# Optimization experiments

Hardware: AMD Instinct MI355X
Metric: run time of the kernel (lower is better)

Reference implementation:

```python
import jax, jax.numpy as jnp
import numpy as np

NODE_DIM = 128
NUM_IRREPS = 224          # 128 + 64 + 32 gates (one per irrep channel)
SPH_DIM = 480             # 128*1 + 64*3 + 32*5
HIDDEN = NODE_DIM + 2 * NUM_IRREPS  # 576
NUM_BASIS = 20
N_NODES = 10000
N_EDGES = 160000
# Each gate scalar is broadcast over its irrep's (2l+1) components.
_REPEATS = np.array([1] * 128 + [3] * 64 + [5] * 32)


def _expand_gate(g):
    # [E, 224] -> [E, 480], repeating each gate over its irrep dimension
    return jnp.repeat(g, _REPEATS, axis=-1, total_repeat_length=SPH_DIM)


def setup_inputs() -> dict:
    key = jax.random.key(0)
    ks = jax.random.split(key, 12)
    x_scalar = jax.random.normal(ks[0], (N_NODES, NODE_DIM), dtype=jnp.float32)
    x_spherical = jax.random.normal(ks[1], (N_NODES, SPH_DIM), dtype=jnp.float32)
    rbf = jax.random.uniform(ks[2], (N_EDGES, NUM_BASIS), dtype=jnp.float32)
    fcut = jax.random.uniform(ks[3], (N_EDGES, 1), dtype=jnp.float32)
    rsh = jax.random.normal(ks[4], (N_EDGES, SPH_DIM), dtype=jnp.float32)
    edge_index = jax.random.randint(ks[5], (2, N_EDGES), 0, N_NODES, dtype=jnp.int64)
    s1 = 1.0 / np.sqrt(NODE_DIM)
    s2 = 1.0 / np.sqrt(NUM_BASIS)
    W1 = jax.random.uniform(ks[6], (NODE_DIM, NODE_DIM), jnp.float32, -s1, s1)
    b1 = jnp.zeros((NODE_DIM,), jnp.float32)
    W2 = jax.random.uniform(ks[7], (NODE_DIM, HIDDEN), jnp.float32, -s1, s1)
    b2 = jnp.zeros((HIDDEN,), jnp.float32)
    Wr = jax.random.uniform(ks[8], (NUM_BASIS, HIDDEN), jnp.float32, -s2, s2)
    br = jnp.zeros((HIDDEN,), jnp.float32)
    return {"x_scalar": x_scalar, "x_spherical": x_spherical, "rbf": rbf,
            "fcut": fcut, "rsh": rsh, "edge_index": edge_index,
            "W1": W1, "b1": b1, "W2": W2, "b2": b2, "Wr": Wr, "br": br}


def reference(x_scalar, x_spherical, rbf, fcut, rsh, edge_index,
              W1, b1, W2, b2, Wr, br):
    src, dst = edge_index[0], edge_index[1]
    # scalar MLP: Linear -> SiLU -> Linear
    scalar_out = jax.nn.silu(x_scalar @ W1 + b1) @ W2 + b2          # [N, 576]
    filter_weight = (rbf @ Wr + br) * fcut                          # [E, 576]
    filter_out = scalar_out[dst] * filter_weight                    # [E, 576]
    gate_state = filter_out[:, :NUM_IRREPS]                         # [E, 224]
    gate_edge = filter_out[:, NUM_IRREPS:2 * NUM_IRREPS]            # [E, 224]
    message_scalar = filter_out[:, 2 * NUM_IRREPS:]                 # [E, 128]
    # ElementwiseTensorProduct(edge_irreps, '224x0e'): per-channel scalar gating
    message_spherical = (x_spherical[dst] * _expand_gate(gate_state)
                         + rsh * _expand_gate(gate_edge))           # [E, 480]
    new_scalar = x_scalar.at[src].add(message_scalar)
    new_spherical = x_spherical.at[src].add(message_spherical)
    return (new_scalar, new_spherical)
```

## Files before the change

kernel.cpp:

```cpp
#include <hip/hip_runtime.h>

#define NODE_DIM 128
#define NUM_IRREPS 224
#define SPH_DIM 480
#define HIDDEN 576
#define NUM_BASIS 20
#define N_NODES 10000
#define N_EDGES 160000
#define NPB 4
#define EB 16
#define NT 36
#define IRP 233
#define SCP 138
#define SOP 577
#define PREP_BLOCKS 2048
#define MLP_BLOCKS ((N_NODES + NPB - 1) / NPB)

typedef __attribute__((ext_vector_type(8))) short short8v;
typedef __attribute__((ext_vector_type(4))) float f32x4;

__device__ __forceinline__ unsigned short f2bf(float f) {
    unsigned int u = __builtin_bit_cast(unsigned int, f);
    u = (u + 0x7fff + ((u >> 16) & 1)) >> 16;
    return (unsigned short)u;
}
__device__ __forceinline__ float bf2f(unsigned short h) {
    unsigned int u = ((unsigned int)h) << 16;
    return __builtin_bit_cast(float, u);
}

__global__ __launch_bounds__(256) void prep_mlp_kernel(
    const float* __restrict__ xs, const float* __restrict__ xsp,
    float* __restrict__ out,
    const int* __restrict__ eidx, int* __restrict__ counts,
    const float* __restrict__ Wr, unsigned short* __restrict__ bfrag,
    const float* __restrict__ W1, const float* __restrict__ b1,
    const float* __restrict__ W2, const float* __restrict__ b2,
    unsigned short* __restrict__ so_bf)
{
    const int t = threadIdx.x;
    if (blockIdx.x < PREP_BLOCKS) {
        const int stride = PREP_BLOCKS * 256;
        const int gt = blockIdx.x * 256 + t;
        for (int i = gt; i < N_NODES * NODE_DIM; i += stride) out[i] = xs[i];
        float* o2 = out + (size_t)N_NODES * NODE_DIM;
        for (int i = gt; i < N_NODES * SPH_DIM; i += stride) o2[i] = xsp[i];
        if (gt < N_EDGES) atomicAdd(&counts[eidx[gt]], 1);
        if (blockIdx.x == PREP_BLOCKS - 1) {
            for (int idx = t; idx < NT * 64; idx += 256) {
                const int nt = idx >> 6, l = idx & 63;
                const int col = nt * 16 + (l & 15);
                const int kb = (l >> 4) * 8;
                #pragma unroll
                for (int j = 0; j < 8; ++j) {
                    const int k = kb + j;
                    bfrag[(size_t)idx * 8 + j] = (k < NUM_BASIS) ? f2bf(Wr[k * HIDDEN + col]) : (unsigned short)0;
                }
            }
        }
        return;
    }
    __shared__ float xsm[NPB][NODE_DIM];
    __shared__ float hsm[NPB][NODE_DIM];
    const int n0 = (blockIdx.x - PREP_BLOCKS) * NPB;
    const int half = t >> 7;
    const int tc = t & 127;

    #pragma unroll
    for (int i = 0; i < 2; ++i) {
        const int nn = 2 * half + i;
        const int node = n0 + nn;
        xsm[nn][tc] = (node < N_NODES) ? xs[(size_t)node * NODE_DIM + tc] : 0.f;
    }
    __syncthreads();

    float acc[2] = {b1[tc], b1[tc]};
    for (int k = 0; k < NODE_DIM; ++k) {
        const float w = W1[k * NODE_DIM + tc];
        #pragma unroll
        for (int i = 0; i < 2; ++i) acc[i] = fmaf(xsm[2 * half + i][k], w, acc[i]);
    }
    #pragma unroll
    for (int i = 0; i < 2; ++i) {
        const float v = acc[i];
        hsm[2 * half + i][tc] = v / (1.f + __expf(-v));
    }
    __syncthreads();

    for (int j = t; j < HIDDEN; j += 256) {
        float a2[NPB];
        #pragma unroll
        for (int n = 0; n < NPB; ++n) a2[n] = b2[j];
        for (int k = 0; k < NODE_DIM; ++k) {
            const float w = W2[k * HIDDEN + j];
            #pragma unroll
            for (int n = 0; n < NPB; ++n) a2[n] = fmaf(hsm[n][k], w, a2[n]);
        }
        #pragma unroll
        for (int n = 0; n < NPB; ++n) {
            const int node = n0 + n;
            if (node < N_NODES) so_bf[(size_t)node * HIDDEN + j] = f2bf(a2[n]);
        }
    }
}

__global__ __launch_bounds__(1024) void scan_kernel(const int* __restrict__ counts,
                                                    int* __restrict__ offsets,
                                                    int* __restrict__ cursor) {
    __shared__ int wsum[16];
    const int tid = threadIdx.x;
    int vals[10];
    int run = 0;
    #pragma unroll
    for (int i = 0; i < 10; ++i) {
        int idx = tid * 10 + i;
        int c = (idx < N_NODES) ? counts[idx] : 0;
        vals[i] = run;
        run += c;
    }
    const int lane = tid & 63, w = tid >> 6;
    int inc = run;
    #pragma unroll
    for (int off = 1; off < 64; off <<= 1) {
        int v = __shfl_up(inc, off);
        if (lane >= off) inc += v;
    }
    if (lane == 63) wsum[w] = inc;
    __syncthreads();
    if (w == 0) {
        int v = (lane < 16) ? wsum[lane] : 0;
        #pragma unroll
        for (int off = 1; off < 16; off <<= 1) {
            int u = __shfl_up(v, off);
            if (lane >= off) v += u;
        }
        if (lane < 16) wsum[lane] = v;
    }
    __syncthreads();
    const int wbase = (w > 0) ? wsum[w - 1] : 0;
    const int base = wbase + inc - run;
    #pragma unroll
    for (int i = 0; i < 10; ++i) {
        int idx = tid * 10 + i;
        if (idx < N_NODES) {
            int v = base + vals[i];
            offsets[idx] = v;
            cursor[idx] = v;
        }
    }
    if (tid == 1023) offsets[N_NODES] = wbase + inc;
}

__global__ __launch_bounds__(256) void scatter_kernel(const int* __restrict__ eidx,
                                                      int* __restrict__ cursor,
                                                      int* __restrict__ edge_order,
                                                      int* __restrict__ edge_src) {
    int i = blockIdx.x * blockDim.x + threadIdx.x;
    if (i < N_EDGES) {
        int s = eidx[i];
        int pos = atomicAdd(&cursor[s], 1);
        edge_order[pos] = i;
        edge_src[pos] = s;
    }
}

__device__ __forceinline__ int gate_of(int d) {
    return (d < 128) ? d : (d < 320) ? (128 + (d - 128) / 3) : (192 + (d - 320) / 5);
}

__global__ __launch_bounds__(256, 4) void edge_mfma(
    const float* __restrict__ xsp,
    const float* __restrict__ rbf, const float* __restrict__ fcut,
    const float* __restrict__ rsh, const int* __restrict__ eidx,
    const unsigned short* __restrict__ bfrag, const float* __restrict__ br,
    const unsigned short* __restrict__ so_bf,
    const int* __restrict__ edge_order, const int* __restrict__ edge_src,
    float* __restrict__ out_scalar, float* __restrict__ out_sph)
{
    __shared__ unsigned short so_s[EB][SOP];
    __shared__ unsigned int   pair_s[EB][IRP];
    __shared__ unsigned short scal_s[EB][SCP];
    __shared__ float rbf_s[EB][NUM_BASIS];
    __shared__ int   e_s[EB];
    __shared__ int   src_s[EB];
    __shared__ int   dst_s[EB];
    __shared__ float fc_s[EB];

    const int t = threadIdx.x;
    const int base = blockIdx.x * EB;
    const int lane = t & 63, w = t >> 6;

    if (t < EB) {
        int pos = base + t;
        int e = edge_order[pos];
        e_s[t]   = e;
        src_s[t] = edge_src[pos];
        dst_s[t] = eidx[N_EDGES + e];
        fc_s[t]  = fcut[e];
    }
    __syncthreads();

    for (int i = t; i < EB * HIDDEN; i += 256) {
        const int row = i / HIDDEN, col = i - row * HIDDEN;
        so_s[row][col] = so_bf[(size_t)dst_s[row] * HIDDEN + col];
    }
    for (int i = t; i < EB * NUM_BASIS; i += 256) {
        const int row = i / NUM_BASIS, k = i - row * NUM_BASIS;
        rbf_s[row][k] = rbf[(size_t)e_s[row] * NUM_BASIS + k];
    }
    __syncthreads();

    const int m_row = lane & 15;
    const int kb = (lane >> 4) * 8;
    short8v a0;
    #pragma unroll
    for (int j = 0; j < 8; ++j) {
        const int k = kb + j;
        a0[j] = (k < NUM_BASIS) ? (short)f2bf(rbf_s[m_row][k]) : (short)0;
    }

    {
        const int rbase = (lane >> 4) * 4;
        float fA[4];
        #pragma unroll
        for (int r = 0; r < 4; ++r) fA[r] = fc_s[rbase + r];
        #pragma unroll
        for (int i = 0; i < NT / 4; ++i) {
            const int nt = w * (NT / 4) + i;
            const short8v bf = *(const short8v*)(bfrag + (size_t)(nt * 64 + lane) * 8);
            f32x4 c0 = {0.f, 0.f, 0.f, 0.f};
            c0 = __builtin_amdgcn_mfma_f32_16x16x32_bf16(a0, bf, c0, 0, 0, 0);
            const int col = nt * 16 + (lane & 15);
            const float brc = br[col];
            #pragma unroll
            for (int r = 0; r < 4; ++r) {
                const int row = rbase + r;
                const float sov = bf2f(so_s[row][col]);
                const float v = (c0[r] + brc) * fA[r] * sov;
                const unsigned short hv = f2bf(v);
                if (col < NUM_IRREPS) {
                    ((unsigned short*)&pair_s[row][col])[0] = hv;
                } else if (col < 2 * NUM_IRREPS) {
                    ((unsigned short*)&pair_s[row][col - NUM_IRREPS])[1] = hv;
                } else {
                    scal_s[row][col - 2 * NUM_IRREPS] = hv;
                }
            }
        }
    }
    __syncthreads();

    const bool sphOn = (t < 240);
    const int d0 = 2 * t;
    const int g0 = sphOn ? gate_of(d0) : 0;
    const int g1 = sphOn ? gate_of(d0 + 1) : 0;

    float accS = 0.f, accD0 = 0.f, accD1 = 0.f;
    int cur_src = src_s[0];

    #pragma unroll
    for (int le = 0; le < EB; ++le) {
        const int s = src_s[le];
        if (s != cur_src) {
            if (sphOn) {
                atomicAdd(&out_sph[(size_t)cur_src * SPH_DIM + d0],     accD0);
                atomicAdd(&out_sph[(size_t)cur_src * SPH_DIM + d0 + 1], accD1);
            }
            if (t < 128) atomicAdd(&out_scalar[(size_t)cur_src * NODE_DIM + t], accS);
            accD0 = accD1 = accS = 0.f;
            cur_src = s;
        }
        if (sphOn) {
            const float2 xv = *(const float2*)(xsp + (size_t)dst_s[le] * SPH_DIM + d0);
            const float2 rv = *(const float2*)(rsh + (size_t)e_s[le]  * SPH_DIM + d0);
            const unsigned int p0 = pair_s[le][g0];
            const unsigned int p1 = pair_s[le][g1];
            accD0 = fmaf(xv.x, bf2f((unsigned short)(p0 & 0xffffu)),
                    fmaf(rv.x, bf2f((unsigned short)(p0 >> 16)), accD0));
            accD1 = fmaf(xv.y, bf2f((unsigned short)(p1 & 0xffffu)),
                    fmaf(rv.y, bf2f((unsigned short)(p1 >> 16)), accD1));
        }
        if (t < 128) accS += bf2f(scal_s[le][t]);
    }
    if (sphOn) {
        atomicAdd(&out_sph[(size_t)cur_src * SPH_DIM + d0],     accD0);
        atomicAdd(&out_sph[(size_t)cur_src * SPH_DIM + d0 + 1], accD1);
    }
    if (t < 128) atomicAdd(&out_scalar[(size_t)cur_src * NODE_DIM + t], accS);
}

extern "C" void kernel_launch(void* const* d_in, const int* in_sizes, int n_in,
                              void* d_out, int out_size, void* d_ws, size_t ws_size,
                              hipStream_t stream) {
    const float* x_scalar    = (const float*)d_in[0];
    const float* x_spherical = (const float*)d_in[1];
    const float* rbf         = (const float*)d_in[2];
    const float* fcut        = (const float*)d_in[3];
    const float* rsh         = (const float*)d_in[4];
    const int*   eidx        = (const int*)d_in[5];
    const float* W1          = (const float*)d_in[6];
    const float* b1          = (const float*)d_in[7];
    const float* W2          = (const float*)d_in[8];
    const float* b2          = (const float*)d_in[9];
    const float* Wr          = (const float*)d_in[10];
    const float* br          = (const float*)d_in[11];

    float* out        = (float*)d_out;
    float* out_scalar = out;
    float* out_sph    = out + (size_t)N_NODES * NODE_DIM;

    unsigned short* so_bf   = (unsigned short*)d_ws;
    int*   counts     = (int*)(so_bf + (size_t)N_NODES * HIDDEN);
    int*   offsets    = counts + N_NODES;
    int*   cursor     = offsets + N_NODES + 1;
    int*   edge_order = cursor + N_NODES;
    int*   edge_src   = edge_order + N_EDGES;
    unsigned short* bfrag = (unsigned short*)((((uintptr_t)(edge_src + N_EDGES)) + 15) & ~(uintptr_t)15);

    hipMemsetAsync(counts, 0, N_NODES * sizeof(int), stream);
    prep_mlp_kernel<<<PREP_BLOCKS + MLP_BLOCKS, 256, 0, stream>>>(
        x_scalar, x_spherical, out, eidx, counts, Wr, bfrag,
        W1, b1, W2, b2, so_bf);
    scan_kernel<<<1, 1024, 0, stream>>>(counts, offsets, cursor);
    scatter_kernel<<<(N_EDGES + 255) / 256, 256, 0, stream>>>(eidx, cursor, edge_order, edge_src);
    edge_mfma<<<N_EDGES / EB, 256, 0, stream>>>(x_spherical, rbf, fcut, rsh, eidx,
                                                bfrag, br, so_bf, edge_order, edge_src,
                                                out_scalar, out_sph);
}
```

Measured before the change: 336.0 us.

## Switch edge kernel to per-node gather, dropping output copy and atomics

```diff
diff --git a/kernel.cpp b/kernel.cpp
--- a/kernel.cpp
+++ b/kernel.cpp
@@ -12,8 +12,7 @@
 #define NT 36
 #define IRP 233
 #define SCP 138
-#define SOP 577
-#define PREP_BLOCKS 2048
+#define PREP_BLOCKS 625
 #define MLP_BLOCKS ((N_NODES + NPB - 1) / NPB)
 
 typedef __attribute__((ext_vector_type(8))) short short8v;
@@ -28,10 +27,12 @@
     unsigned int u = ((unsigned int)h) << 16;
     return __builtin_bit_cast(float, u);
 }
+__device__ __forceinline__ int gate_of(int d) {
+    return (d < 128) ? d : (d < 320) ? (128 + (d - 128) / 3) : (192 + (d - 320) / 5);
+}
 
 __global__ __launch_bounds__(256) void prep_mlp_kernel(
-    const float* __restrict__ xs, const float* __restrict__ xsp,
-    float* __restrict__ out,
+    const float* __restrict__ xs,
     const int* __restrict__ eidx, int* __restrict__ counts,
     const float* __restrict__ Wr, unsigned short* __restrict__ bfrag,
     const float* __restrict__ W1, const float* __restrict__ b1,
@@ -40,11 +41,7 @@
 {
     const int t = threadIdx.x;
     if (blockIdx.x < PREP_BLOCKS) {
-        const int stride = PREP_BLOCKS * 256;
         const int gt = blockIdx.x * 256 + t;
-        for (int i = gt; i < N_NODES * NODE_DIM; i += stride) out[i] = xs[i];
-        float* o2 = out + (size_t)N_NODES * NODE_DIM;
-        for (int i = gt; i < N_NODES * SPH_DIM; i += stride) o2[i] = xsp[i];
         if (gt < N_EDGES) atomicAdd(&counts[eidx[gt]], 1);
         if (blockIdx.x == PREP_BLOCKS - 1) {
             for (int idx = t; idx < NT * 64; idx += 256) {
@@ -153,102 +150,34 @@
 
 __global__ __launch_bounds__(256) void scatter_kernel(const int* __restrict__ eidx,
                                                       int* __restrict__ cursor,
-                                                      int* __restrict__ edge_order,
-                                                      int* __restrict__ edge_src) {
+                                                      int* __restrict__ edge_order) {
     int i = blockIdx.x * blockDim.x + threadIdx.x;
     if (i < N_EDGES) {
         int s = eidx[i];
         int pos = atomicAdd(&cursor[s], 1);
         edge_order[pos] = i;
-        edge_src[pos] = s;
-    }
-}
-
-__device__ __forceinline__ int gate_of(int d) {
-    return (d < 128) ? d : (d < 320) ? (128 + (d - 128) / 3) : (192 + (d - 320) / 5);
-}
-
-__global__ __launch_bounds__(256, 4) void edge_mfma(
-    const float* __restrict__ xsp,
+    }
+}
+
+__global__ __launch_bounds__(256, 4) void node_mfma(
+    const float* __restrict__ xs, const float* __restrict__ xsp,
     const float* __restrict__ rbf, const float* __restrict__ fcut,
     const float* __restrict__ rsh, const int* __restrict__ eidx,
     const unsigned short* __restrict__ bfrag, const float* __restrict__ br,
     const unsigned short* __restrict__ so_bf,
-    const int* __restrict__ edge_order, const int* __restrict__ edge_src,
+    const int* __restrict__ offsets, const int* __restrict__ edge_order,
     float* __restrict__ out_scalar, float* __restrict__ out_sph)
 {
-    __shared__ unsigned short so_s[EB][SOP];
     __shared__ unsigned int   pair_s[EB][IRP];
     __shared__ unsigned short scal_s[EB][SCP];
-    __shared__ float rbf_s[EB][NUM_BASIS];
     __shared__ int   e_s[EB];
-    __shared__ int   src_s[EB];
     __shared__ int   dst_s[EB];
     __shared__ float fc_s[EB];
 
     const int t = threadIdx.x;
-    const int base = blockIdx.x * EB;
+    const int n = blockIdx.x;
     const int lane = t & 63, w = t >> 6;
-
-    if (t < EB) {
-        int pos = base + t;
-        int e = edge_order[pos];
-        e_s[t]   = e;
-        src_s[t] = edge_src[pos];
-        dst_s[t] = eidx[N_EDGES + e];
-        fc_s[t]  = fcut[e];
-    }
-    __syncthreads();
-
-    for (int i = t; i < EB * HIDDEN; i += 256) {
-        const int row = i / HIDDEN, col = i - row * HIDDEN;
-        so_s[row][col] = so_bf[(size_t)dst_s[row] * HIDDEN + col];
-    }
-    for (int i = t; i < EB * NUM_BASIS; i += 256) {
-        const int row = i / NUM_BASIS, k = i - row * NUM_BASIS;
-        rbf_s[row][k] = rbf[(size_t)e_s[row] * NUM_BASIS + k];
-    }
-    __syncthreads();
-
-    const int m_row = lane & 15;
-    const int kb = (lane >> 4) * 8;
-    short8v a0;
-    #pragma unroll
-    for (int j = 0; j < 8; ++j) {
-        const int k = kb + j;
-        a0[j] = (k < NUM_BASIS) ? (short)f2bf(rbf_s[m_row][k]) : (short)0;
-    }
-
-    {
-        const int rbase = (lane >> 4) * 4;
-        float fA[4];
-        #pragma unroll
-        for (int r = 0; r < 4; ++r) fA[r] = fc_s[rbase + r];
-        #pragma unroll
-        for (int i = 0; i < NT / 4; ++i) {
-            const int nt = w * (NT / 4) + i;
-            const short8v bf = *(const short8v*)(bfrag + (size_t)(nt * 64 + lane) * 8);
-            f32x4 c0 = {0.f, 0.f, 0.f, 0.f};
-            c0 = __builtin_amdgcn_mfma_f32_16x16x32_bf16(a0, bf, c0, 0, 0, 0);
-            const int col = nt * 16 + (lane & 15);
-            const float brc = br[col];
-            #pragma unroll
-            for (int r = 0; r < 4; ++r) {
-                const int row = rbase + r;
-                const float sov = bf2f(so_s[row][col]);
-                const float v = (c0[r] + brc) * fA[r] * sov;
-                const unsigned short hv = f2bf(v);
-                if (col < NUM_IRREPS) {
-                    ((unsigned short*)&pair_s[row][col])[0] = hv;
-                } else if (col < 2 * NUM_IRREPS) {
-                    ((unsigned short*)&pair_s[row][col - NUM_IRREPS])[1] = hv;
-                } else {
-                    scal_s[row][col - 2 * NUM_IRREPS] = hv;
-                }
-            }
-        }
-    }
-    __syncthreads();
+    const int beg = offsets[n], end_ = offsets[n + 1];
 
     const bool sphOn = (t < 240);
     const int d0 = 2 * t;
@@ -256,37 +185,99 @@
     const int g1 = sphOn ? gate_of(d0 + 1) : 0;
 
     float accS = 0.f, accD0 = 0.f, accD1 = 0.f;
-    int cur_src = src_s[0];
-
-    #pragma unroll
-    for (int le = 0; le < EB; ++le) {
-        const int s = src_s[le];
-        if (s != cur_src) {
+
+    for (int chunk = beg; chunk < end_; chunk += EB) {
+        const int cnt = min(EB, end_ - chunk);
+        if (t < EB) {
+            if (t < cnt) {
+                const int e = edge_order[chunk + t];
+                e_s[t]   = e;
+                dst_s[t] = eidx[N_EDGES + e];
+                fc_s[t]  = fcut[e];
+            } else {
+                e_s[t] = 0; dst_s[t] = 0; fc_s[t] = 0.f;
+            }
+        }
+        __syncthreads();
+
+        const int m_row = lane & 15;
+        const int kb = (lane >> 4) * 8;
+        short8v a0;
+        {
+            const int er = edge_order[chunk + min(m_row, cnt - 1)];
+            const float* rrow = rbf + (size_t)er * NUM_BASIS;
+            float q[8];
+            if (kb < 16) {
+                const float4 v0 = *(const float4*)(rrow + kb);
+                const float4 v1 = *(const float4*)(rrow + kb + 4);
+                q[0]=v0.x; q[1]=v0.y; q[2]=v0.z; q[3]=v0.w;
+                q[4]=v1.x; q[5]=v1.y; q[6]=v1.z; q[7]=v1.w;
+            } else if (kb == 16) {
+                const float4 v0 = *(const float4*)(rrow + 16);
+                q[0]=v0.x; q[1]=v0.y; q[2]=v0.z; q[3]=v0.w;
+                q[4]=0.f; q[5]=0.f; q[6]=0.f; q[7]=0.f;
+            } else {
+                #pragma unroll
+                for (int j = 0; j < 8; ++j) q[j] = 0.f;
+            }
+            #pragma unroll
+            for (int j = 0; j < 8; ++j) a0[j] = (short)f2bf(q[j]);
+        }
+
+        {
+            const int rbase = (lane >> 4) * 4;
+            int dA[4]; float fA[4];
+            #pragma unroll
+            for (int r = 0; r < 4; ++r) { dA[r] = dst_s[rbase + r]; fA[r] = fc_s[rbase + r]; }
+            #pragma unroll
+            for (int i = 0; i < NT / 4; ++i) {
+                const int nt = w * (NT / 4) + i;
+                const short8v bf = *(const short8v*)(bfrag + (size_t)(nt * 64 + lane) * 8);
+                f32x4 c0 = {0.f, 0.f, 0.f, 0.f};
+                c0 = __builtin_amdgcn_mfma_f32_16x16x32_bf16(a0, bf, c0, 0, 0, 0);
+                const int col = nt * 16 + (lane & 15);
+                const float brc = br[col];
+                #pragma unroll
+                for (int r = 0; r < 4; ++r) {
+                    const int row = rbase + r;
+                    const float sov = bf2f(so_bf[(size_t)dA[r] * HIDDEN + col]);
+                    const float v = (c0[r] + brc) * fA[r] * sov;
+                    const unsigned short hv = f2bf(v);
+                    if (col < NUM_IRREPS) {
+                        ((unsigned short*)&pair_s[row][col])[0] = hv;
+                    } else if (col < 2 * NUM_IRREPS) {
+                        ((unsigned short*)&pair_s[row][col - NUM_IRREPS])[1] = hv;
+                    } else {
+                        scal_s[row][col - 2 * NUM_IRREPS] = hv;
+                    }
+                }
+            }
+        }
+        __syncthreads();
+
+        for (int le = 0; le < cnt; ++le) {
             if (sphOn) {
-                atomicAdd(&out_sph[(size_t)cur_src * SPH_DIM + d0],     accD0);
-                atomicAdd(&out_sph[(size_t)cur_src * SPH_DIM + d0 + 1], accD1);
-            }
-            if (t < 128) atomicAdd(&out_scalar[(size_t)cur_src * NODE_DIM + t], accS);
-            accD0 = accD1 = accS = 0.f;
-            cur_src = s;
-        }
-        if (sphOn) {
-            const float2 xv = *(const float2*)(xsp + (size_t)dst_s[le] * SPH_DIM + d0);
-            const float2 rv = *(const float2*)(rsh + (size_t)e_s[le]  * SPH_DIM + d0);
-            const unsigned int p0 = pair_s[le][g0];
-            const unsigned int p1 = pair_s[le][g1];
-            accD0 = fmaf(xv.x, bf2f((unsigned short)(p0 & 0xffffu)),
-                    fmaf(rv.x, bf2f((unsigned short)(p0 >> 16)), accD0));
-            accD1 = fmaf(xv.y, bf2f((unsigned short)(p1 & 0xffffu)),
-                    fmaf(rv.y, bf2f((unsigned short)(p1 >> 16)), accD1));
-        }
-        if (t < 128) accS += bf2f(scal_s[le][t]);
-    }
+                const float2 xv = *(const float2*)(xsp + (size_t)dst_s[le] * SPH_DIM + d0);
+                const float2 rv = *(const float2*)(rsh + (size_t)e_s[le]  * SPH_DIM + d0);
+                const unsigned int p0 = pair_s[le][g0];
+                const unsigned int p1 = pair_s[le][g1];
+                accD0 = fmaf(xv.x, bf2f((unsigned short)(p0 & 0xffffu)),
+                        fmaf(rv.x, bf2f((unsigned short)(p0 >> 16)), accD0));
+                accD1 = fmaf(xv.y, bf2f((unsigned short)(p1 & 0xffffu)),
+                        fmaf(rv.y, bf2f((unsigned short)(p1 >> 16)), accD1));
+            }
+            if (t < 128) accS += bf2f(scal_s[le][t]);
+        }
+        __syncthreads();
+    }
+
+    if (t < 128)
+        out_scalar[(size_t)n * NODE_DIM + t] = xs[(size_t)n * NODE_DIM + t] + accS;
     if (sphOn) {
-        atomicAdd(&out_sph[(size_t)cur_src * SPH_DIM + d0],     accD0);
-        atomicAdd(&out_sph[(size_t)cur_src * SPH_DIM + d0 + 1], accD1);
-    }
-    if (t < 128) atomicAdd(&out_scalar[(size_t)cur_src * NODE_DIM + t], accS);
+        const float2 xv = *(const float2*)(xsp + (size_t)n * SPH_DIM + d0);
+        float2 o; o.x = xv.x + accD0; o.y = xv.y + accD1;
+        *(float2*)(out_sph + (size_t)n * SPH_DIM + d0) = o;
+    }
 }
 
 extern "C" void kernel_launch(void* const* d_in, const int* in_sizes, int n_in,
@@ -309,21 +300,19 @@
     float* out_scalar = out;
     float* out_sph    = out + (size_t)N_NODES * NODE_DIM;
 
-    unsigned short* so_bf   = (unsigned short*)d_ws;
+    unsigned short* so_bf = (unsigned short*)d_ws;
     int*   counts     = (int*)(so_bf + (size_t)N_NODES * HIDDEN);
     int*   offsets    = counts + N_NODES;
     int*   cursor     = offsets + N_NODES + 1;
     int*   edge_order = cursor + N_NODES;
-    int*   edge_src   = edge_order + N_EDGES;
-    unsigned short* bfrag = (unsigned short*)((((uintptr_t)(edge_src + N_EDGES)) + 15) & ~(uintptr_t)15);
+    unsigned short* bfrag = (unsigned short*)((((uintptr_t)(edge_order + N_EDGES)) + 15) & ~(uintptr_t)15);
 
     hipMemsetAsync(counts, 0, N_NODES * sizeof(int), stream);
     prep_mlp_kernel<<<PREP_BLOCKS + MLP_BLOCKS, 256, 0, stream>>>(
-        x_scalar, x_spherical, out, eidx, counts, Wr, bfrag,
-        W1, b1, W2, b2, so_bf);
+        x_scalar, eidx, counts, Wr, bfrag, W1, b1, W2, b2, so_bf);
     scan_kernel<<<1, 1024, 0, stream>>>(counts, offsets, cursor);
-    scatter_kernel<<<(N_EDGES + 255) / 256, 256, 0, stream>>>(eidx, cursor, edge_order, edge_src);
-    edge_mfma<<<N_EDGES / EB, 256, 0, stream>>>(x_spherical, rbf, fcut, rsh, eidx,
-                                                bfrag, br, so_bf, edge_order, edge_src,
-                                                out_scalar, out_sph);
-}
+    scatter_kernel<<<(N_EDGES + 255) / 256, 256, 0, stream>>>(eidx, cursor, edge_order);
+    node_mfma<<<N_NODES, 256, 0, stream>>>(x_scalar, x_spherical, rbf, fcut, rsh, eidx,
+                                           bfrag, br, so_bf, offsets, edge_order,
+                                           out_scalar, out_sph);
+}
```

New measurement: 542.5 us. 61.4% more time.

## Replace atomic scatter with per-window bf16 partials and a deterministic finalize pass

Applied to the files above, without the earlier changes.

```diff
diff --git a/kernel.cpp b/kernel.cpp
--- a/kernel.cpp
+++ b/kernel.cpp
@@ -9,11 +9,13 @@
 #define N_EDGES 160000
 #define NPB 4
 #define EB 16
+#define NWIN (N_EDGES / EB)
 #define NT 36
 #define IRP 233
 #define SCP 138
-#define SOP 577
-#define PREP_BLOCKS 2048
+#define PROW 608
+#define MAXP 20480
+#define PREP_BLOCKS 625
 #define MLP_BLOCKS ((N_NODES + NPB - 1) / NPB)
 
 typedef __attribute__((ext_vector_type(8))) short short8v;
@@ -28,10 +30,12 @@
     unsigned int u = ((unsigned int)h) << 16;
     return __builtin_bit_cast(float, u);
 }
+__device__ __forceinline__ int gate_of(int d) {
+    return (d < 128) ? d : (d < 320) ? (128 + (d - 128) / 3) : (192 + (d - 320) / 5);
+}
 
 __global__ __launch_bounds__(256) void prep_mlp_kernel(
-    const float* __restrict__ xs, const float* __restrict__ xsp,
-    float* __restrict__ out,
+    const float* __restrict__ xs,
     const int* __restrict__ eidx, int* __restrict__ counts,
     const float* __restrict__ Wr, unsigned short* __restrict__ bfrag,
     const float* __restrict__ W1, const float* __restrict__ b1,
@@ -40,11 +44,7 @@
 {
     const int t = threadIdx.x;
     if (blockIdx.x < PREP_BLOCKS) {
-        const int stride = PREP_BLOCKS * 256;
         const int gt = blockIdx.x * 256 + t;
-        for (int i = gt; i < N_NODES * NODE_DIM; i += stride) out[i] = xs[i];
-        float* o2 = out + (size_t)N_NODES * NODE_DIM;
-        for (int i = gt; i < N_NODES * SPH_DIM; i += stride) o2[i] = xsp[i];
         if (gt < N_EDGES) atomicAdd(&counts[eidx[gt]], 1);
         if (blockIdx.x == PREP_BLOCKS - 1) {
             for (int idx = t; idx < NT * 64; idx += 256) {
@@ -106,19 +106,21 @@
 
 __global__ __launch_bounds__(1024) void scan_kernel(const int* __restrict__ counts,
                                                     int* __restrict__ offsets,
-                                                    int* __restrict__ cursor) {
+                                                    int* __restrict__ cursor,
+                                                    int* __restrict__ pairbase) {
     __shared__ int wsum[16];
     const int tid = threadIdx.x;
-    int vals[10];
+    const int lane = tid & 63, w = tid >> 6;
+    int deg[10], vals[10];
+
     int run = 0;
     #pragma unroll
     for (int i = 0; i < 10; ++i) {
         int idx = tid * 10 + i;
-        int c = (idx < N_NODES) ? counts[idx] : 0;
+        deg[i] = (idx < N_NODES) ? counts[idx] : 0;
         vals[i] = run;
-        run += c;
-    }
-    const int lane = tid & 63, w = tid >> 6;
+        run += deg[i];
+    }
     int inc = run;
     #pragma unroll
     for (int off = 1; off < 64; off <<= 1) {
@@ -139,16 +141,53 @@
     __syncthreads();
     const int wbase = (w > 0) ? wsum[w - 1] : 0;
     const int base = wbase + inc - run;
+    int off_n[10];
     #pragma unroll
     for (int i = 0; i < 10; ++i) {
         int idx = tid * 10 + i;
+        off_n[i] = base + vals[i];
         if (idx < N_NODES) {
-            int v = base + vals[i];
-            offsets[idx] = v;
-            cursor[idx] = v;
+            offsets[idx] = off_n[i];
+            cursor[idx] = off_n[i];
         }
     }
     if (tid == 1023) offsets[N_NODES] = wbase + inc;
+    __syncthreads();
+
+    int run2 = 0;
+    int vals2[10];
+    #pragma unroll
+    for (int i = 0; i < 10; ++i) {
+        int wins = (deg[i] > 0) ? (((off_n[i] + deg[i] - 1) >> 4) - (off_n[i] >> 4) + 1) : 0;
+        vals2[i] = run2;
+        run2 += wins;
+    }
+    int inc2 = run2;
+    #pragma unroll
+    for (int off = 1; off < 64; off <<= 1) {
+        int v = __shfl_up(inc2, off);
+        if (lane >= off) inc2 += v;
+    }
+    if (lane == 63) wsum[w] = inc2;
+    __syncthreads();
+    if (w == 0) {
+        int v = (lane < 16) ? wsum[lane] : 0;
+        #pragma unroll
+        for (int off = 1; off < 16; off <<= 1) {
+            int u = __shfl_up(v, off);
+            if (lane >= off) v += u;
+        }
+        if (lane < 16) wsum[lane] = v;
+    }
+    __syncthreads();
+    const int wbase2 = (w > 0) ? wsum[w - 1] : 0;
+    const int base2 = wbase2 + inc2 - run2;
+    #pragma unroll
+    for (int i = 0; i < 10; ++i) {
+        int idx = tid * 10 + i;
+        if (idx < N_NODES) pairbase[idx] = base2 + vals2[i];
+    }
+    if (tid == 1023) pairbase[N_NODES] = wbase2 + inc2;
 }
 
 __global__ __launch_bounds__(256) void scatter_kernel(const int* __restrict__ eidx,
@@ -164,10 +203,6 @@
     }
 }
 
-__device__ __forceinline__ int gate_of(int d) {
-    return (d < 128) ? d : (d < 320) ? (128 + (d - 128) / 3) : (192 + (d - 320) / 5);
-}
-
 __global__ __launch_bounds__(256, 4) void edge_mfma(
     const float* __restrict__ xsp,
     const float* __restrict__ rbf, const float* __restrict__ fcut,
@@ -175,55 +210,55 @@
     const unsigned short* __restrict__ bfrag, const float* __restrict__ br,
     const unsigned short* __restrict__ so_bf,
     const int* __restrict__ edge_order, const int* __restrict__ edge_src,
-    float* __restrict__ out_scalar, float* __restrict__ out_sph)
+    const int* __restrict__ offsets, const int* __restrict__ pairbase,
+    unsigned short* __restrict__ partials)
 {
-    __shared__ unsigned short so_s[EB][SOP];
     __shared__ unsigned int   pair_s[EB][IRP];
     __shared__ unsigned short scal_s[EB][SCP];
-    __shared__ float rbf_s[EB][NUM_BASIS];
     __shared__ int   e_s[EB];
     __shared__ int   src_s[EB];
     __shared__ int   dst_s[EB];
+    __shared__ int   off_s[EB];
+    __shared__ int   pb_s[EB];
     __shared__ float fc_s[EB];
 
     const int t = threadIdx.x;
-    const int base = blockIdx.x * EB;
+    const int win = blockIdx.x;
+    const int base = win * EB;
     const int lane = t & 63, w = t >> 6;
+
+    const int m_row = lane & 15;
+    const int kb = (lane >> 4) * 8;
+    const int e_row = edge_order[base + m_row];
+    short8v a0;
+    {
+        const float* rrow = rbf + (size_t)e_row * NUM_BASIS;
+        #pragma unroll
+        for (int j = 0; j < 8; ++j) {
+            const int k = kb + j;
+            a0[j] = (k < NUM_BASIS) ? (short)f2bf(rrow[k]) : (short)0;
+        }
+    }
 
     if (t < EB) {
         int pos = base + t;
         int e = edge_order[pos];
+        int s = edge_src[pos];
         e_s[t]   = e;
-        src_s[t] = edge_src[pos];
+        src_s[t] = s;
         dst_s[t] = eidx[N_EDGES + e];
         fc_s[t]  = fcut[e];
-    }
-    __syncthreads();
-
-    for (int i = t; i < EB * HIDDEN; i += 256) {
-        const int row = i / HIDDEN, col = i - row * HIDDEN;
-        so_s[row][col] = so_bf[(size_t)dst_s[row] * HIDDEN + col];
-    }
-    for (int i = t; i < EB * NUM_BASIS; i += 256) {
-        const int row = i / NUM_BASIS, k = i - row * NUM_BASIS;
-        rbf_s[row][k] = rbf[(size_t)e_s[row] * NUM_BASIS + k];
-    }
-    __syncthreads();
-
-    const int m_row = lane & 15;
-    const int kb = (lane >> 4) * 8;
-    short8v a0;
-    #pragma unroll
-    for (int j = 0; j < 8; ++j) {
-        const int k = kb + j;
-        a0[j] = (k < NUM_BASIS) ? (short)f2bf(rbf_s[m_row][k]) : (short)0;
-    }
+        off_s[t] = offsets[s];
+        pb_s[t]  = pairbase[s];
+    }
+    __syncthreads();
 
     {
         const int rbase = (lane >> 4) * 4;
+        int   dA[4];
         float fA[4];
         #pragma unroll
-        for (int r = 0; r < 4; ++r) fA[r] = fc_s[rbase + r];
+        for (int r = 0; r < 4; ++r) { dA[r] = dst_s[rbase + r]; fA[r] = fc_s[rbase + r]; }
         #pragma unroll
         for (int i = 0; i < NT / 4; ++i) {
             const int nt = w * (NT / 4) + i;
@@ -235,7 +270,7 @@
             #pragma unroll
             for (int r = 0; r < 4; ++r) {
                 const int row = rbase + r;
-                const float sov = bf2f(so_s[row][col]);
+                const float sov = bf2f(so_bf[(size_t)dA[r] * HIDDEN + col]);
                 const float v = (c0[r] + brc) * fA[r] * sov;
                 const unsigned short hv = f2bf(v);
                 if (col < NUM_IRREPS) {
@@ -256,19 +291,20 @@
     const int g1 = sphOn ? gate_of(d0 + 1) : 0;
 
     float accS = 0.f, accD0 = 0.f, accD1 = 0.f;
-    int cur_src = src_s[0];
+    int cur = 0;
 
     #pragma unroll
     for (int le = 0; le < EB; ++le) {
-        const int s = src_s[le];
-        if (s != cur_src) {
+        if (src_s[le] != src_s[cur]) {
+            const int prow = pb_s[cur] + (win - (off_s[cur] >> 4));
+            unsigned short* pr = partials + (size_t)prow * PROW;
+            if (t < 128) pr[t] = f2bf(accS);
             if (sphOn) {
-                atomicAdd(&out_sph[(size_t)cur_src * SPH_DIM + d0],     accD0);
-                atomicAdd(&out_sph[(size_t)cur_src * SPH_DIM + d0 + 1], accD1);
+                pr[NODE_DIM + d0]     = f2bf(accD0);
+                pr[NODE_DIM + d0 + 1] = f2bf(accD1);
             }
-            if (t < 128) atomicAdd(&out_scalar[(size_t)cur_src * NODE_DIM + t], accS);
             accD0 = accD1 = accS = 0.f;
-            cur_src = s;
+            cur = le;
         }
         if (sphOn) {
             const float2 xv = *(const float2*)(xsp + (size_t)dst_s[le] * SPH_DIM + d0);
@@ -282,11 +318,45 @@
         }
         if (t < 128) accS += bf2f(scal_s[le][t]);
     }
+    {
+        const int prow = pb_s[cur] + (win - (off_s[cur] >> 4));
+        unsigned short* pr = partials + (size_t)prow * PROW;
+        if (t < 128) pr[t] = f2bf(accS);
+        if (sphOn) {
+            pr[NODE_DIM + d0]     = f2bf(accD0);
+            pr[NODE_DIM + d0 + 1] = f2bf(accD1);
+        }
+    }
+}
+
+__global__ __launch_bounds__(256) void finalize_kernel(
+    const float* __restrict__ xs, const float* __restrict__ xsp,
+    const unsigned short* __restrict__ partials,
+    const int* __restrict__ pairbase,
+    float* __restrict__ out_scalar, float* __restrict__ out_sph)
+{
+    const int t = threadIdx.x;
+    const int n = blockIdx.x;
+    const int pb = pairbase[n], pe = pairbase[n + 1];
+    const bool sphOn = (t < 240);
+    const int d0 = 2 * t;
+
+    float accS = 0.f, a0 = 0.f, a1 = 0.f;
+    for (int p = pb; p < pe; ++p) {
+        const unsigned short* pr = partials + (size_t)p * PROW;
+        if (t < 128) accS += bf2f(pr[t]);
+        if (sphOn) {
+            a0 += bf2f(pr[NODE_DIM + d0]);
+            a1 += bf2f(pr[NODE_DIM + d0 + 1]);
+        }
+    }
+    if (t < 128)
+        out_scalar[(size_t)n * NODE_DIM + t] = xs[(size_t)n * NODE_DIM + t] + accS;
     if (sphOn) {
-        atomicAdd(&out_sph[(size_t)cur_src * SPH_DIM + d0],     accD0);
-        atomicAdd(&out_sph[(size_t)cur_src * SPH_DIM + d0 + 1], accD1);
-    }
-    if (t < 128) atomicAdd(&out_scalar[(size_t)cur_src * NODE_DIM + t], accS);
+        const float2 xv = *(const float2*)(xsp + (size_t)n * SPH_DIM + d0);
+        float2 o; o.x = xv.x + a0; o.y = xv.y + a1;
+        *(float2*)(out_sph + (size_t)n * SPH_DIM + d0) = o;
+    }
 }
 
 extern "C" void kernel_launch(void* const* d_in, const int* in_sizes, int n_in,
@@ -309,21 +379,24 @@
     float* out_scalar = out;
     float* out_sph    = out + (size_t)N_NODES * NODE_DIM;
 
-    unsigned short* so_bf   = (unsigned short*)d_ws;
-    int*   counts     = (int*)(so_bf + (size_t)N_NODES * HIDDEN);
+    unsigned short* so_bf = (unsigned short*)d_ws;
+    unsigned short* partials = so_bf + (size_t)N_NODES * HIDDEN;
+    int*   counts     = (int*)(partials + (size_t)MAXP * PROW);
     int*   offsets    = counts + N_NODES;
-    int*   cursor     = offsets + N_NODES + 1;
+    int*   pairbase   = offsets + N_NODES + 1;
+    int*   cursor     = pairbase + N_NODES + 1;
     int*   edge_order = cursor + N_NODES;
     int*   edge_src   = edge_order + N_EDGES;
     unsigned short* bfrag = (unsigned short*)((((uintptr_t)(edge_src + N_EDGES)) + 15) & ~(uintptr_t)15);
 
     hipMemsetAsync(counts, 0, N_NODES * sizeof(int), stream);
     prep_mlp_kernel<<<PREP_BLOCKS + MLP_BLOCKS, 256, 0, stream>>>(
-        x_scalar, x_spherical, out, eidx, counts, Wr, bfrag,
-        W1, b1, W2, b2, so_bf);
-    scan_kernel<<<1, 1024, 0, stream>>>(counts, offsets, cursor);
+        x_scalar, eidx, counts, Wr, bfrag, W1, b1, W2, b2, so_bf);
+    scan_kernel<<<1, 1024, 0, stream>>>(counts, offsets, cursor, pairbase);
     scatter_kernel<<<(N_EDGES + 255) / 256, 256, 0, stream>>>(eidx, cursor, edge_order, edge_src);
-    edge_mfma<<<N_EDGES / EB, 256, 0, stream>>>(x_spherical, rbf, fcut, rsh, eidx,
-                                                bfrag, br, so_bf, edge_order, edge_src,
-                                                out_scalar, out_sph);
-}
+    edge_mfma<<<NWIN, 256, 0, stream>>>(x_spherical, rbf, fcut, rsh, eidx,
+                                        bfrag, br, so_bf, edge_order, edge_src,
+                                        offsets, pairbase, partials);
+    finalize_kernel<<<N_NODES, 256, 0, stream>>>(x_scalar, x_spherical, partials, pairbase,
+                                                 out_scalar, out_sph);
+}
```

New measurement: 294.4 us. 1.14x faster.
